# Optimization experiments

Hardware: AMD Instinct MI355X
Metric: run time of the kernel (lower is better)

Reference implementation:

```python
import jax, jax.numpy as jnp
import numpy as np

B, T_D, T_P = 64, 256, 1024
DRUG_DIM, PROT_DIM, D = 128, 128, 128
MAX_LEN = 1024
NEG = -1e9


def _linear_params(k, out_d, in_d):
    k1, k2 = jax.random.split(k)
    lim = 1.0 / np.sqrt(in_d)
    W = jax.random.uniform(k1, (out_d, in_d), minval=-lim, maxval=lim, dtype=jnp.float32)
    b = jax.random.uniform(k2, (out_d,), minval=-lim, maxval=lim, dtype=jnp.float32)
    return W, b


def setup_inputs() -> dict:
    key = jax.random.key(0)
    ks = jax.random.split(key, 13)
    inp = {
        'smiles_embeddings': jax.random.normal(ks[0], (B, T_D, DRUG_DIM), dtype=jnp.float32),
        'protein_embeddings': jax.random.normal(ks[1], (B, T_P, PROT_DIM), dtype=jnp.float32),
        'smiles_mask': jax.random.randint(ks[2], (B, T_D), 0, 2, dtype=jnp.int32),
        'protein_mask': jax.random.randint(ks[3], (B, T_P), 0, 2, dtype=jnp.int32),
        # torch inits pos_bias to zeros; small random values make the test nontrivial
        'pos_bias': 0.02 * jax.random.normal(ks[4], (MAX_LEN, MAX_LEN), dtype=jnp.float32),
    }
    names = [('Wqd', 'bqd', DRUG_DIM), ('Wkp', 'bkp', PROT_DIM), ('Wvp', 'bvp', PROT_DIM),
             ('Wqp', 'bqp', PROT_DIM), ('Wkd', 'bkd', DRUG_DIM), ('Wvd', 'bvd', DRUG_DIM),
             ('Wpd', 'bpd', D), ('Wpp', 'bpp', D)]
    for i, (wn, bn, in_d) in enumerate(names):
        W, b = _linear_params(ks[5 + i], D, in_d)
        inp[wn] = W
        inp[bn] = b
    return inp


def _lin(x, W, b):
    return x @ W.T + b


def _aft(q, k, v, pb_masked, Wp, bp):
    # q: [B,Ti,D]; k,v: [B,Tj,D]; pb_masked: [B,Ti,Tj]
    max_k = k.max(axis=1, keepdims=True)              # per (b,d) over seq j
    max_pb = pb_masked.max(axis=2, keepdims=True)     # per (b,i) over j
    exp_k = jnp.exp(k - max_k)                        # [B,Tj,D]
    exp_pb = jnp.exp(pb_masked - max_pb)              # [B,Ti,Tj]
    num = jnp.einsum('bij,bjd->bid', exp_pb, exp_k * v)
    den = jnp.einsum('bij,bjd->bid', exp_pb, exp_k)
    y = jax.nn.sigmoid(q) * num / den
    return _lin(y, Wp, bp)


def reference(smiles_embeddings, protein_embeddings, smiles_mask, protein_mask, pos_bias,
              Wqd, bqd, Wkp, bkp, Wvp, bvp, Wqp, bqp, Wkd, bkd, Wvd, bvd, Wpd, bpd, Wpp, bpp):
    Td = smiles_embeddings.shape[1]
    Tp = protein_embeddings.shape[1]
    combined = smiles_mask[:, :, None] * protein_mask[:, None, :]  # [B,Td,Tp]
    pb = pos_bias[:Td, :Tp][None]                                   # [1,Td,Tp]

    # drug queries attend over protein keys/values
    pb_d = jnp.where(combined == 0, NEG, pb)
    y_d = _aft(_lin(smiles_embeddings, Wqd, bqd),
               _lin(protein_embeddings, Wkp, bkp),
               _lin(protein_embeddings, Wvp, bvp), pb_d, Wpd, bpd)

    # protein queries attend over drug keys/values (transposed pos bias)
    pb_p = jnp.where(jnp.swapaxes(combined, 1, 2) == 0, NEG, jnp.swapaxes(pb, 1, 2))
    y_p = _aft(_lin(protein_embeddings, Wqp, bqp),
               _lin(smiles_embeddings, Wkd, bkd),
               _lin(smiles_embeddings, Wvd, bvd), pb_p, Wpp, bpp)

    y_d = jnp.where(smiles_mask[:, :, None] == 0, NEG, y_d).max(axis=1)   # [B,D]
    y_p = jnp.where(protein_mask[:, :, None] == 0, NEG, y_p).max(axis=1)  # [B,D]
    return y_d, y_p
```

## Files before the change

kernel.cpp:

```cpp
#include <hip/hip_runtime.h>
#include <cstdint>
#include <cstddef>

#define NEGV -1e9f

typedef __bf16 bf16x8 __attribute__((ext_vector_type(8)));
typedef float f32x4 __attribute__((ext_vector_type(4)));
typedef unsigned short us4 __attribute__((ext_vector_type(4)));
typedef unsigned short us8 __attribute__((ext_vector_type(8)));

__device__ __forceinline__ unsigned short f2bf(float f) {
  unsigned int u = __float_as_uint(f);
  u += 0x7fffu + ((u >> 16) & 1u);
  return (unsigned short)(u >> 16);
}
__device__ __forceinline__ float bf2f(unsigned short u) {
  return __uint_as_float(((unsigned)u) << 16);
}

__device__ __forceinline__ void gld16(const void* g, void* l) {
  __builtin_amdgcn_global_load_lds(
      (const __attribute__((address_space(1))) unsigned int*)g,
      (__attribute__((address_space(3))) unsigned int*)l, 16, 0, 0);
}

__global__ void prep_kernel(const float* __restrict__ w0, const float* __restrict__ w1,
                            const float* __restrict__ w2, const float* __restrict__ w3,
                            const float* __restrict__ w4, const float* __restrict__ w5,
                            const float* __restrict__ w6, const float* __restrict__ w7,
                            unsigned short* __restrict__ Wbf,
                            const float* __restrict__ pb,
                            unsigned short* __restrict__ epb,
                            unsigned short* __restrict__ epbT,
                            unsigned int* __restrict__ outEnc) {
  __shared__ unsigned short t[32][33];
  const int blk = blockIdx.x, tid = threadIdx.x;
  if (blk < 64) {
    outEnc[blk * 256 + tid] = 0u;
    return;
  }
  if (blk < 192) {
    const float* Ws[8] = {w0, w1, w2, w3, w4, w5, w6, w7};
    int idx = (blk - 64) * 256 + tid;
    int mat = idx >> 12, off = idx & 4095;
    float4 v = *(const float4*)&Ws[mat][(size_t)off * 4];
    us4 p;
    p.x = f2bf(v.x); p.y = f2bf(v.y); p.z = f2bf(v.z); p.w = f2bf(v.w);
    *(us4*)&Wbf[(size_t)mat * 16384 + (size_t)off * 4] = p;
    return;
  }
  const int bid = blk - 192;
  const int j0 = (bid & 31) * 32, i0 = (bid >> 5) * 32;
  const int tx = tid & 31, ty = tid >> 5;
#pragma unroll
  for (int r = 0; r < 4; ++r) {
    int i = i0 + ty + r * 8;
    unsigned short u = f2bf(__expf(pb[(size_t)i * 1024 + j0 + tx]));
    epb[(size_t)i * 1024 + j0 + tx] = u;
    t[ty + r * 8][tx] = u;
  }
  __syncthreads();
#pragma unroll
  for (int r = 0; r < 4; ++r)
    epbT[(size_t)(j0 + ty + r * 8) * 256 + i0 + tx] = t[tx][ty + r * 8];
}

__global__ __launch_bounds__(256) void proj3_all(
    const float* __restrict__ smiles, const float* __restrict__ prot,
    const int* __restrict__ smask, const int* __restrict__ pmask,
    const unsigned short* __restrict__ Wbf,
    const float* __restrict__ bqd, const float* __restrict__ bkd, const float* __restrict__ bvd,
    const float* __restrict__ bqp, const float* __restrict__ bkp, const float* __restrict__ bvp,
    unsigned short* __restrict__ sigQd, unsigned short* __restrict__ eKTd,
    unsigned short* __restrict__ eKVTd,
    unsigned short* __restrict__ sigQp, unsigned short* __restrict__ eKTp,
    unsigned short* __restrict__ eKVTp) {
  __shared__ unsigned short smem[2 * 128 * 72];
  unsigned short* xL = smem;
  const int tid = threadIdx.x;

  const float* X; const int* mask;
  const unsigned short *Wq, *Wk, *Wv;
  const float *bq, *bk_, *bv;
  unsigned short *sigQ, *eKT, *eKVT;
  int T, g0;
  if (blockIdx.x < 256) {
    X = smiles; mask = smask; T = 256; g0 = blockIdx.x * 64;
    Wq = Wbf; Wk = Wbf + 16384; Wv = Wbf + 32768;
    bq = bqd; bk_ = bkd; bv = bvd;
    sigQ = sigQd; eKT = eKTd; eKVT = eKVTd;
  } else {
    X = prot; mask = pmask; T = 1024; g0 = (blockIdx.x - 256) * 64;
    Wq = Wbf + 3 * 16384; Wk = Wbf + 4 * 16384; Wv = Wbf + 5 * 16384;
    bq = bqp; bk_ = bkp; bv = bvp;
    sigQ = sigQp; eKT = eKTp; eKVT = eKVTp;
  }
  const int b = g0 / T;
  const int tl0 = g0 - b * T;

#pragma unroll
  for (int r = 0; r < 8; ++r) {
    int i4 = tid + 256 * r;
    int t = i4 >> 5, k4 = (i4 & 31) * 4;
    float4 v = *(const float4*)&X[(size_t)(g0 + t) * 128 + k4];
    us4 p;
    p.x = f2bf(v.x); p.y = f2bf(v.y); p.z = f2bf(v.z); p.w = f2bf(v.w);
    *(us4*)&xL[t * 136 + k4] = p;
  }
  __syncthreads();

  const int lane = tid & 63, wave = tid >> 6;
  const int lo = lane & 15, hi = lane >> 4;
  const int d0 = wave * 32;

  f32x4 aQ[4][2], aK[4][2], aV[4][2];
#pragma unroll
  for (int a = 0; a < 4; ++a)
#pragma unroll
    for (int s = 0; s < 2; ++s)
#pragma unroll
      for (int r = 0; r < 4; ++r) { aQ[a][s][r] = 0.f; aK[a][s][r] = 0.f; aV[a][s][r] = 0.f; }

#pragma unroll
  for (int kt = 0; kt < 128; kt += 32) {
    bf16x8 bQ[2], bK[2], bV[2];
#pragma unroll
    for (int s = 0; s < 2; ++s) {
      size_t roff = (size_t)(d0 + s * 16 + lo) * 128 + kt + hi * 8;
      bQ[s] = *(const bf16x8*)&Wq[roff];
      bK[s] = *(const bf16x8*)&Wk[roff];
      bV[s] = *(const bf16x8*)&Wv[roff];
    }
#pragma unroll
    for (int a = 0; a < 4; ++a) {
      bf16x8 af = *(const bf16x8*)&xL[(a * 16 + lo) * 136 + kt + hi * 8];
#pragma unroll
      for (int s = 0; s < 2; ++s) {
        aQ[a][s] = __builtin_amdgcn_mfma_f32_16x16x32_bf16(af, bQ[s], aQ[a][s], 0, 0, 0);
        aK[a][s] = __builtin_amdgcn_mfma_f32_16x16x32_bf16(af, bK[s], aK[a][s], 0, 0, 0);
        aV[a][s] = __builtin_amdgcn_mfma_f32_16x16x32_bf16(af, bV[s], aV[a][s], 0, 0, 0);
      }
    }
  }

#pragma unroll
  for (int s = 0; s < 2; ++s) {
    int d = d0 + s * 16 + lo;
    float bb = bq[d];
#pragma unroll
    for (int a = 0; a < 4; ++a)
#pragma unroll
      for (int r = 0; r < 4; ++r) {
        int t = g0 + a * 16 + hi * 4 + r;
        float q = aQ[a][s][r] + bb;
        sigQ[(size_t)t * 128 + d] = f2bf(1.f / (1.f + __expf(-q)));
      }
  }

  __syncthreads();
  unsigned short* ekL = smem;
  unsigned short* ekvL = smem + 9216;
#pragma unroll
  for (int s = 0; s < 2; ++s) {
    int d = d0 + s * 16 + lo;
    float bbk = bk_[d], bbv = bv[d];
#pragma unroll
    for (int a = 0; a < 4; ++a)
#pragma unroll
      for (int r = 0; r < 4; ++r) {
        int tl = a * 16 + hi * 4 + r;
        int mk = mask[g0 + tl];
        float ek = mk ? __expf(aK[a][s][r] + bbk) : 0.f;
        float ekv = ek * (aV[a][s][r] + bbv);
        ekL[d * 72 + tl] = f2bf(ek);
        ekvL[d * 72 + tl] = f2bf(ekv);
      }
  }
  __syncthreads();
#pragma unroll
  for (int r = 0; r < 8; ++r) {
    int q = tid + 256 * r;
    int arr = q >> 10, qq = q & 1023;
    int d = qq >> 3, c = qq & 7;
    us8 v = *(const us8*)&smem[arr * 9216 + d * 72 + c * 8];
    unsigned short* dst = arr ? eKVT : eKT;
    *(us8*)&dst[((size_t)b * 128 + d) * T + tl0 + c * 8] = v;
  }
}

__global__ __launch_bounds__(256, 2) void aft_all(
    const unsigned short* __restrict__ epb, const unsigned short* __restrict__ epbT,
    const unsigned short* __restrict__ eKTd, const unsigned short* __restrict__ eKVTd,
    const unsigned short* __restrict__ eKTp, const unsigned short* __restrict__ eKVTp,
    const unsigned short* __restrict__ sigQd, const unsigned short* __restrict__ sigQp,
    const int* __restrict__ smask, const int* __restrict__ pmask,
    const unsigned short* __restrict__ Wbf,
    const float* __restrict__ bpd, const float* __restrict__ bpp,
    unsigned int* __restrict__ outEnc) {
  __shared__ unsigned short smem[32768];

  const int blk = blockIdx.x;
  const unsigned short *Ap, *KT, *VT, *SQ, *Wp;
  const float* bp;
  const int* msk;
  unsigned int* oEnc;
  int b, i0, TJ, Ti, astr;
  if (blk < 128) {
    b = blk & 63; i0 = (blk >> 6) * 128; TJ = 1024; Ti = 256;
    Ap = epb; astr = 1024; KT = eKTp; VT = eKVTp; SQ = sigQd;
    Wp = Wbf + 6 * 16384; bp = bpd; msk = smask + b * 256 + i0; oEnc = outEnc;
  } else {
    int k = blk - 128;
    b = k & 63; i0 = (k >> 6) * 128; TJ = 256; Ti = 1024;
    Ap = epbT; astr = 256; KT = eKTd; VT = eKVTd; SQ = sigQp;
    Wp = Wbf + 7 * 16384; bp = bpp; msk = pmask + b * 1024 + i0; oEnc = outEnc + 8192;
  }

  const int tid = threadIdx.x, lane = tid & 63, w = tid >> 6;
  const int lo = lane & 15, hi = lane >> 4;
  const int wi = (w >> 1) * 64, wd = (w & 1) * 64;
  const unsigned short* KTb = KT + (size_t)b * 128 * TJ;
  const unsigned short* VTb = VT + (size_t)b * 128 * TJ;
  const int slotbase = w * 256;

  auto stage = [&](int jt, int p) {
    unsigned short* bkL = smem + p * 16384;
    unsigned short* bvL = bkL + 8192;
#pragma unroll
    for (int it = 0; it < 4; ++it) {
      int slot = slotbase + it * 64 + lane;
      int r = slot >> 3, sc = slot & 7;
      int cg = sc ^ (r & 7);
      size_t goff = (size_t)r * TJ + jt + cg * 8;
      gld16(KTb + goff, &bkL[(slotbase + it * 64) * 8]);
      gld16(VTb + goff, &bvL[(slotbase + it * 64) * 8]);
    }
  };

  f32x4 aN[4][4], aD[4][4];
#pragma unroll
  for (int a = 0; a < 4; ++a)
#pragma unroll
    for (int n = 0; n < 4; ++n)
#pragma unroll
      for (int r = 0; r < 4; ++r) { aN[a][n][r] = 0.f; aD[a][n][r] = 0.f; }

  stage(0, 0);
  bf16x8 af_cur[4][2];
#pragma unroll
  for (int a = 0; a < 4; ++a)
#pragma unroll
    for (int kt = 0; kt < 2; ++kt)
      af_cur[a][kt] = *(const bf16x8*)
          &Ap[(size_t)(i0 + wi + a * 16 + lo) * astr + kt * 32 + hi * 8];

  int p = 0;
  for (int jt = 0; jt < TJ; jt += 64) {
    const int jn = (jt + 64 < TJ) ? jt + 64 : jt;
    stage(jn, p ^ 1);
    bf16x8 af_nxt[4][2];
#pragma unroll
    for (int a = 0; a < 4; ++a)
#pragma unroll
      for (int kt = 0; kt < 2; ++kt)
        af_nxt[a][kt] = *(const bf16x8*)
            &Ap[(size_t)(i0 + wi + a * 16 + lo) * astr + jn + kt * 32 + hi * 8];
    asm volatile("s_waitcnt vmcnt(16)\ns_barrier" ::: "memory");

    const unsigned short* bkL = smem + p * 16384;
    const unsigned short* bvL = bkL + 8192;
#pragma unroll
    for (int kt = 0; kt < 2; ++kt) {
      bf16x8 bk[4], bv[4];
#pragma unroll
      for (int n = 0; n < 4; ++n) {
        int row = wd + n * 16 + lo;
        int sc = ((kt * 4 + hi) ^ (row & 7)) * 8;
        bk[n] = *(const bf16x8*)&bkL[row * 64 + sc];
        bv[n] = *(const bf16x8*)&bvL[row * 64 + sc];
      }
#pragma unroll
      for (int a = 0; a < 4; ++a)
#pragma unroll
        for (int n = 0; n < 4; ++n) {
          aN[a][n] = __builtin_amdgcn_mfma_f32_16x16x32_bf16(af_cur[a][kt], bv[n], aN[a][n], 0, 0, 0);
          aD[a][n] = __builtin_amdgcn_mfma_f32_16x16x32_bf16(af_cur[a][kt], bk[n], aD[a][n], 0, 0, 0);
        }
    }
    asm volatile("s_waitcnt lgkmcnt(0)\ns_barrier" ::: "memory");
#pragma unroll
    for (int a = 0; a < 4; ++a)
#pragma unroll
      for (int kt = 0; kt < 2; ++kt)
        af_cur[a][kt] = af_nxt[a][kt];
    p ^= 1;
  }

  __syncthreads();
  unsigned short* yL = smem;
#pragma unroll
  for (int a = 0; a < 4; ++a)
#pragma unroll
    for (int n = 0; n < 4; ++n) {
      int iL = wi + a * 16 + hi * 4;
      int d = wd + n * 16 + lo;
#pragma unroll
      for (int r = 0; r < 4; ++r) {
        size_t off = ((size_t)b * Ti + i0 + iL + r) * 128 + d;
        float s = bf2f(SQ[off]);
        float y = s * __fdividef(aN[a][n][r], aD[a][n][r]);
        yL[(iL + r) * 136 + d] = f2bf(y);
      }
    }
  __syncthreads();

  f32x4 aZ[4][4];
#pragma unroll
  for (int a = 0; a < 4; ++a)
#pragma unroll
    for (int n = 0; n < 4; ++n)
#pragma unroll
      for (int r = 0; r < 4; ++r) aZ[a][n][r] = 0.f;

#pragma unroll
  for (int kt = 0; kt < 128; kt += 32) {
    bf16x8 bw[4];
#pragma unroll
    for (int n = 0; n < 4; ++n)
      bw[n] = *(const bf16x8*)&Wp[(size_t)(wd + n * 16 + lo) * 128 + kt + hi * 8];
#pragma unroll
    for (int a = 0; a < 4; ++a) {
      bf16x8 af = *(const bf16x8*)&yL[(wi + a * 16 + lo) * 136 + kt + hi * 8];
#pragma unroll
      for (int n = 0; n < 4; ++n)
        aZ[a][n] = __builtin_amdgcn_mfma_f32_16x16x32_bf16(af, bw[n], aZ[a][n], 0, 0, 0);
    }
  }

#pragma unroll
  for (int n = 0; n < 4; ++n) {
    int d = wd + n * 16 + lo;
    float bb = bp[d];
    float m = NEGV;
#pragma unroll
    for (int a = 0; a < 4; ++a)
#pragma unroll
      for (int r = 0; r < 4; ++r) {
        int iL = wi + a * 16 + hi * 4 + r;
        float z = aZ[a][n][r] + bb;
        m = msk[iL] ? fmaxf(m, z) : m;
      }
    m = fmaxf(m, __shfl_xor(m, 16, 64));
    m = fmaxf(m, __shfl_xor(m, 32, 64));
    if (hi == 0) {
      unsigned bits = __float_as_uint(m);
      unsigned key = (bits & 0x80000000u) ? ~bits : (bits | 0x80000000u);
      atomicMax(&oEnc[b * 128 + d], key);
    }
  }
}

__global__ void out_decode(unsigned int* o) {
  int i = blockIdx.x * 256 + threadIdx.x;
  unsigned k = o[i];
  unsigned bits = (k & 0x80000000u) ? (k ^ 0x80000000u) : ~k;
  ((float*)o)[i] = __uint_as_float(bits);
}

extern "C" void kernel_launch(void* const* d_in, const int* in_sizes, int n_in,
                              void* d_out, int out_size, void* d_ws, size_t ws_size,
                              hipStream_t stream) {
  const float* smiles = (const float*)d_in[0];
  const float* prot   = (const float*)d_in[1];
  const int* smask = (const int*)d_in[2];
  const int* pmask = (const int*)d_in[3];
  const float* pos_bias = (const float*)d_in[4];
  const float* Wqd = (const float*)d_in[5];  const float* bqd = (const float*)d_in[6];
  const float* Wkp = (const float*)d_in[7];  const float* bkp = (const float*)d_in[8];
  const float* Wvp = (const float*)d_in[9];  const float* bvp = (const float*)d_in[10];
  const float* Wqp = (const float*)d_in[11]; const float* bqp = (const float*)d_in[12];
  const float* Wkd = (const float*)d_in[13]; const float* bkd = (const float*)d_in[14];
  const float* Wvd = (const float*)d_in[15]; const float* bvd = (const float*)d_in[16];
  const float* Wpd = (const float*)d_in[17]; const float* bpd = (const float*)d_in[18];
  const float* Wpp = (const float*)d_in[19]; const float* bpp = (const float*)d_in[20];

  unsigned short* u = (unsigned short*)d_ws;
  unsigned short* eKTp  = u;
  unsigned short* eKVTp = eKTp + 8388608;
  unsigned short* eKTd  = eKVTp + 8388608;
  unsigned short* eKVTd = eKTd + 2097152;
  unsigned short* sigQd = eKVTd + 2097152;
  unsigned short* sigQp = sigQd + 2097152;
  unsigned short* epb_  = sigQp + 8388608;
  unsigned short* epbT_ = epb_ + 262144;
  unsigned short* Wbf   = epbT_ + 262144;

  dim3 blk(256);

  prep_kernel<<<448, blk, 0, stream>>>(Wqd, Wkd, Wvd, Wqp, Wkp, Wvp, Wpd, Wpp,
                                       Wbf, pos_bias, epb_, epbT_,
                                       (unsigned int*)d_out);

  proj3_all<<<1280, blk, 0, stream>>>(smiles, prot, smask, pmask, Wbf,
                                      bqd, bkd, bvd, bqp, bkp, bvp,
                                      sigQd, eKTd, eKVTd, sigQp, eKTp, eKVTp);

  aft_all<<<640, blk, 0, stream>>>(epb_, epbT_, eKTd, eKVTd, eKTp, eKVTp,
                                   sigQd, sigQp, smask, pmask, Wbf,
                                   bpd, bpp, (unsigned int*)d_out);

  out_decode<<<64, blk, 0, stream>>>((unsigned int*)d_out);
}
```

Measured before the change: 196.5 us.

## Pre-swizzle operands into MFMA fragment layout and drop LDS staging in AFT

The projection kernel now writes sigmoid(Q), exp(K) and exp(K)*V directly in MFMA-fragment-ordered layouts, and extra blocks reorder the exp(pos_bias) matrices the same way. The AFT kernel then loads each operand fragment straight from global memory with contiguous 16-byte loads. This replaces the double-buffered LDS pipeline with its barriers and the LDS transpose pass in the projection kernel. The cost is that the main loop no longer overlaps prefetch explicitly and relies on cache and occupancy to hide global latency. B fragments are also re-read from global memory by each wave instead of being shared through LDS.

```diff
diff --git a/kernel.cpp b/kernel.cpp
--- a/kernel.cpp
+++ b/kernel.cpp
@@ -18,11 +18,6 @@
   return __uint_as_float(((unsigned)u) << 16);
 }
 
-__device__ __forceinline__ void gld16(const void* g, void* l) {
-  __builtin_amdgcn_global_load_lds(
-      (const __attribute__((address_space(1))) unsigned int*)g,
-      (__attribute__((address_space(3))) unsigned int*)l, 16, 0, 0);
-}
 
 __global__ void prep_kernel(const float* __restrict__ w0, const float* __restrict__ w1,
                             const float* __restrict__ w2, const float* __restrict__ w3,
@@ -71,32 +66,50 @@
     const unsigned short* __restrict__ Wbf,
     const float* __restrict__ bqd, const float* __restrict__ bkd, const float* __restrict__ bvd,
     const float* __restrict__ bqp, const float* __restrict__ bkp, const float* __restrict__ bvp,
-    unsigned short* __restrict__ sigQd, unsigned short* __restrict__ eKTd,
-    unsigned short* __restrict__ eKVTd,
-    unsigned short* __restrict__ sigQp, unsigned short* __restrict__ eKTp,
-    unsigned short* __restrict__ eKVTp) {
-  __shared__ unsigned short smem[2 * 128 * 72];
-  unsigned short* xL = smem;
+    const unsigned short* __restrict__ epb, const unsigned short* __restrict__ epbT,
+    unsigned short* __restrict__ AFd, unsigned short* __restrict__ AFp,
+    unsigned short* __restrict__ SQd, unsigned short* __restrict__ BKd,
+    unsigned short* __restrict__ BVd,
+    unsigned short* __restrict__ SQp, unsigned short* __restrict__ BKp,
+    unsigned short* __restrict__ BVp) {
   const int tid = threadIdx.x;
+
+  if (blockIdx.x >= 1280) {
+    int sid = (blockIdx.x - 1280) * 256 + tid;
+    if (sid < 32768) {
+      int lane = sid & 63, kt = (sid >> 6) & 31, it = sid >> 11;
+      int i = it * 16 + (lane & 15), j = kt * 32 + (lane >> 4) * 8;
+      *(us8*)&AFd[(size_t)sid * 8] = *(const us8*)&epb[(size_t)i * 1024 + j];
+    } else {
+      int s2 = sid - 32768;
+      int lane = s2 & 63, kt = (s2 >> 6) & 7, it = s2 >> 9;
+      int i = it * 16 + (lane & 15), j = kt * 32 + (lane >> 4) * 8;
+      *(us8*)&AFp[(size_t)s2 * 8] = *(const us8*)&epbT[(size_t)i * 256 + j];
+    }
+    return;
+  }
+
+  __shared__ unsigned short xL[64 * 136];
 
   const float* X; const int* mask;
   const unsigned short *Wq, *Wk, *Wv;
   const float *bq, *bk_, *bv;
-  unsigned short *sigQ, *eKT, *eKVT;
+  unsigned short *SQ, *BK, *BV;
   int T, g0;
   if (blockIdx.x < 256) {
     X = smiles; mask = smask; T = 256; g0 = blockIdx.x * 64;
     Wq = Wbf; Wk = Wbf + 16384; Wv = Wbf + 32768;
     bq = bqd; bk_ = bkd; bv = bvd;
-    sigQ = sigQd; eKT = eKTd; eKVT = eKVTd;
+    SQ = SQd; BK = BKd; BV = BVd;
   } else {
     X = prot; mask = pmask; T = 1024; g0 = (blockIdx.x - 256) * 64;
     Wq = Wbf + 3 * 16384; Wk = Wbf + 4 * 16384; Wv = Wbf + 5 * 16384;
     bq = bqp; bk_ = bkp; bv = bvp;
-    sigQ = sigQp; eKT = eKTp; eKVT = eKVTp;
+    SQ = SQp; BK = BKp; BV = BVp;
   }
   const int b = g0 / T;
   const int tl0 = g0 - b * T;
+  const int NIT = T / 16, NKT = T / 32;
 
 #pragma unroll
   for (int r = 0; r < 8; ++r) {
@@ -145,97 +158,83 @@
 
 #pragma unroll
   for (int s = 0; s < 2; ++s) {
-    int d = d0 + s * 16 + lo;
-    float bb = bq[d];
-#pragma unroll
-    for (int a = 0; a < 4; ++a)
+    int dt = (d0 >> 4) + s;
+    float bb = bq[d0 + s * 16 + lo];
+#pragma unroll
+    for (int a = 0; a < 4; ++a) {
+      int it = (tl0 >> 4) + a;
+      us4 v;
 #pragma unroll
       for (int r = 0; r < 4; ++r) {
-        int t = g0 + a * 16 + hi * 4 + r;
         float q = aQ[a][s][r] + bb;
-        sigQ[(size_t)t * 128 + d] = f2bf(1.f / (1.f + __expf(-q)));
-      }
-  }
-
-  __syncthreads();
-  unsigned short* ekL = smem;
-  unsigned short* ekvL = smem + 9216;
+        v[r] = f2bf(1.f / (1.f + __expf(-q)));
+      }
+      ((us4*)SQ)[(((size_t)b * NIT + it) * 8 + dt) * 64 + lane] = v;
+    }
+  }
+
 #pragma unroll
   for (int s = 0; s < 2; ++s) {
-    int d = d0 + s * 16 + lo;
-    float bbk = bk_[d], bbv = bv[d];
-#pragma unroll
-    for (int a = 0; a < 4; ++a)
+    int dt = (d0 >> 4) + s;
+    float bbk = bk_[d0 + s * 16 + lo], bbv = bv[d0 + s * 16 + lo];
+#pragma unroll
+    for (int a = 0; a < 4; ++a) {
+      int kt = (tl0 >> 5) + (a >> 1);
+      int lane_f = ((a & 1) * 2 + (hi >> 1)) * 16 + lo;
+      us4 vk, vv;
 #pragma unroll
       for (int r = 0; r < 4; ++r) {
-        int tl = a * 16 + hi * 4 + r;
-        int mk = mask[g0 + tl];
+        int tg = g0 + a * 16 + hi * 4 + r;
+        int mk = mask[tg];
         float ek = mk ? __expf(aK[a][s][r] + bbk) : 0.f;
         float ekv = ek * (aV[a][s][r] + bbv);
-        ekL[d * 72 + tl] = f2bf(ek);
-        ekvL[d * 72 + tl] = f2bf(ekv);
-      }
-  }
-  __syncthreads();
-#pragma unroll
-  for (int r = 0; r < 8; ++r) {
-    int q = tid + 256 * r;
-    int arr = q >> 10, qq = q & 1023;
-    int d = qq >> 3, c = qq & 7;
-    us8 v = *(const us8*)&smem[arr * 9216 + d * 72 + c * 8];
-    unsigned short* dst = arr ? eKVT : eKT;
-    *(us8*)&dst[((size_t)b * 128 + d) * T + tl0 + c * 8] = v;
+        vk[r] = f2bf(ek);
+        vv[r] = f2bf(ekv);
+      }
+      size_t q4 = ((((size_t)b * NKT + kt) * 8 + dt) * 64 + lane_f) * 2 + (hi & 1);
+      ((us4*)BK)[q4] = vk;
+      ((us4*)BV)[q4] = vv;
+    }
   }
 }
 
 __global__ __launch_bounds__(256, 2) void aft_all(
-    const unsigned short* __restrict__ epb, const unsigned short* __restrict__ epbT,
-    const unsigned short* __restrict__ eKTd, const unsigned short* __restrict__ eKVTd,
-    const unsigned short* __restrict__ eKTp, const unsigned short* __restrict__ eKVTp,
-    const unsigned short* __restrict__ sigQd, const unsigned short* __restrict__ sigQp,
+    const unsigned short* __restrict__ AFd, const unsigned short* __restrict__ AFp,
+    const unsigned short* __restrict__ SQd, const unsigned short* __restrict__ BKd,
+    const unsigned short* __restrict__ BVd,
+    const unsigned short* __restrict__ SQp, const unsigned short* __restrict__ BKp,
+    const unsigned short* __restrict__ BVp,
     const int* __restrict__ smask, const int* __restrict__ pmask,
     const unsigned short* __restrict__ Wbf,
     const float* __restrict__ bpd, const float* __restrict__ bpp,
     unsigned int* __restrict__ outEnc) {
-  __shared__ unsigned short smem[32768];
+  __shared__ unsigned short yL[128 * 136];
 
   const int blk = blockIdx.x;
-  const unsigned short *Ap, *KT, *VT, *SQ, *Wp;
+  const unsigned short *AF, *BK, *BV, *SQ, *Wp;
   const float* bp;
   const int* msk;
   unsigned int* oEnc;
-  int b, i0, TJ, Ti, astr;
+  int b, i0, NKT, NIT;
   if (blk < 128) {
-    b = blk & 63; i0 = (blk >> 6) * 128; TJ = 1024; Ti = 256;
-    Ap = epb; astr = 1024; KT = eKTp; VT = eKVTp; SQ = sigQd;
+    b = blk & 63; i0 = (blk >> 6) * 128; NKT = 32; NIT = 16;
+    AF = AFd; BK = BKp; BV = BVp; SQ = SQd;
     Wp = Wbf + 6 * 16384; bp = bpd; msk = smask + b * 256 + i0; oEnc = outEnc;
   } else {
     int k = blk - 128;
-    b = k & 63; i0 = (k >> 6) * 128; TJ = 256; Ti = 1024;
-    Ap = epbT; astr = 256; KT = eKTd; VT = eKVTd; SQ = sigQp;
+    b = k & 63; i0 = (k >> 6) * 128; NKT = 8; NIT = 64;
+    AF = AFp; BK = BKd; BV = BVd; SQ = SQp;
     Wp = Wbf + 7 * 16384; bp = bpp; msk = pmask + b * 1024 + i0; oEnc = outEnc + 8192;
   }
 
   const int tid = threadIdx.x, lane = tid & 63, w = tid >> 6;
   const int lo = lane & 15, hi = lane >> 4;
   const int wi = (w >> 1) * 64, wd = (w & 1) * 64;
-  const unsigned short* KTb = KT + (size_t)b * 128 * TJ;
-  const unsigned short* VTb = VT + (size_t)b * 128 * TJ;
-  const int slotbase = w * 256;
-
-  auto stage = [&](int jt, int p) {
-    unsigned short* bkL = smem + p * 16384;
-    unsigned short* bvL = bkL + 8192;
-#pragma unroll
-    for (int it = 0; it < 4; ++it) {
-      int slot = slotbase + it * 64 + lane;
-      int r = slot >> 3, sc = slot & 7;
-      int cg = sc ^ (r & 7);
-      size_t goff = (size_t)r * TJ + jt + cg * 8;
-      gld16(KTb + goff, &bkL[(slotbase + it * 64) * 8]);
-      gld16(VTb + goff, &bvL[(slotbase + it * 64) * 8]);
-    }
-  };
+  const int it0 = (i0 + wi) >> 4;
+  const int dt0 = wd >> 4;
+
+  const unsigned short* BKb = BK + (size_t)b * NKT * 8 * 64 * 8;
+  const unsigned short* BVb = BV + (size_t)b * NKT * 8 * 64 * 8;
 
   f32x4 aN[4][4], aD[4][4];
 #pragma unroll
@@ -245,70 +244,38 @@
 #pragma unroll
       for (int r = 0; r < 4; ++r) { aN[a][n][r] = 0.f; aD[a][n][r] = 0.f; }
 
-  stage(0, 0);
-  bf16x8 af_cur[4][2];
+#pragma unroll 2
+  for (int kt = 0; kt < NKT; ++kt) {
+    bf16x8 af[4];
+#pragma unroll
+    for (int a = 0; a < 4; ++a)
+      af[a] = *(const bf16x8*)&AF[(((size_t)(it0 + a) * NKT + kt) * 64 + lane) * 8];
+    bf16x8 bk[4], bv[4];
+#pragma unroll
+    for (int n = 0; n < 4; ++n) {
+      size_t x = (((size_t)kt * 8 + dt0 + n) * 64 + lane) * 8;
+      bk[n] = *(const bf16x8*)&BKb[x];
+      bv[n] = *(const bf16x8*)&BVb[x];
+    }
+#pragma unroll
+    for (int a = 0; a < 4; ++a)
+#pragma unroll
+      for (int n = 0; n < 4; ++n) {
+        aN[a][n] = __builtin_amdgcn_mfma_f32_16x16x32_bf16(af[a], bv[n], aN[a][n], 0, 0, 0);
+        aD[a][n] = __builtin_amdgcn_mfma_f32_16x16x32_bf16(af[a], bk[n], aD[a][n], 0, 0, 0);
+      }
+  }
+
 #pragma unroll
   for (int a = 0; a < 4; ++a)
 #pragma unroll
-    for (int kt = 0; kt < 2; ++kt)
-      af_cur[a][kt] = *(const bf16x8*)
-          &Ap[(size_t)(i0 + wi + a * 16 + lo) * astr + kt * 32 + hi * 8];
-
-  int p = 0;
-  for (int jt = 0; jt < TJ; jt += 64) {
-    const int jn = (jt + 64 < TJ) ? jt + 64 : jt;
-    stage(jn, p ^ 1);
-    bf16x8 af_nxt[4][2];
-#pragma unroll
-    for (int a = 0; a < 4; ++a)
-#pragma unroll
-      for (int kt = 0; kt < 2; ++kt)
-        af_nxt[a][kt] = *(const bf16x8*)
-            &Ap[(size_t)(i0 + wi + a * 16 + lo) * astr + jn + kt * 32 + hi * 8];
-    asm volatile("s_waitcnt vmcnt(16)\ns_barrier" ::: "memory");
-
-    const unsigned short* bkL = smem + p * 16384;
-    const unsigned short* bvL = bkL + 8192;
-#pragma unroll
-    for (int kt = 0; kt < 2; ++kt) {
-      bf16x8 bk[4], bv[4];
-#pragma unroll
-      for (int n = 0; n < 4; ++n) {
-        int row = wd + n * 16 + lo;
-        int sc = ((kt * 4 + hi) ^ (row & 7)) * 8;
-        bk[n] = *(const bf16x8*)&bkL[row * 64 + sc];
-        bv[n] = *(const bf16x8*)&bvL[row * 64 + sc];
-      }
-#pragma unroll
-      for (int a = 0; a < 4; ++a)
-#pragma unroll
-        for (int n = 0; n < 4; ++n) {
-          aN[a][n] = __builtin_amdgcn_mfma_f32_16x16x32_bf16(af_cur[a][kt], bv[n], aN[a][n], 0, 0, 0);
-          aD[a][n] = __builtin_amdgcn_mfma_f32_16x16x32_bf16(af_cur[a][kt], bk[n], aD[a][n], 0, 0, 0);
-        }
-    }
-    asm volatile("s_waitcnt lgkmcnt(0)\ns_barrier" ::: "memory");
-#pragma unroll
-    for (int a = 0; a < 4; ++a)
-#pragma unroll
-      for (int kt = 0; kt < 2; ++kt)
-        af_cur[a][kt] = af_nxt[a][kt];
-    p ^= 1;
-  }
-
-  __syncthreads();
-  unsigned short* yL = smem;
-#pragma unroll
-  for (int a = 0; a < 4; ++a)
-#pragma unroll
     for (int n = 0; n < 4; ++n) {
+      us4 q = ((const us4*)SQ)[(((size_t)b * NIT + it0 + a) * 8 + dt0 + n) * 64 + lane];
       int iL = wi + a * 16 + hi * 4;
       int d = wd + n * 16 + lo;
 #pragma unroll
       for (int r = 0; r < 4; ++r) {
-        size_t off = ((size_t)b * Ti + i0 + iL + r) * 128 + d;
-        float s = bf2f(SQ[off]);
-        float y = s * __fdividef(aN[a][n][r], aD[a][n][r]);
+        float y = bf2f(q[r]) * __fdividef(aN[a][n][r], aD[a][n][r]);
         yL[(iL + r) * 136 + d] = f2bf(y);
       }
     }
@@ -385,15 +352,17 @@
   const float* Wpp = (const float*)d_in[19]; const float* bpp = (const float*)d_in[20];
 
   unsigned short* u = (unsigned short*)d_ws;
-  unsigned short* eKTp  = u;
-  unsigned short* eKVTp = eKTp + 8388608;
-  unsigned short* eKTd  = eKVTp + 8388608;
-  unsigned short* eKVTd = eKTd + 2097152;
-  unsigned short* sigQd = eKVTd + 2097152;
-  unsigned short* sigQp = sigQd + 2097152;
-  unsigned short* epb_  = sigQp + 8388608;
+  unsigned short* BKp_  = u;
+  unsigned short* BVp_  = BKp_ + 8388608;
+  unsigned short* BKd_  = BVp_ + 8388608;
+  unsigned short* BVd_  = BKd_ + 2097152;
+  unsigned short* SQd_  = BVd_ + 2097152;
+  unsigned short* SQp_  = SQd_ + 2097152;
+  unsigned short* epb_  = SQp_ + 8388608;
   unsigned short* epbT_ = epb_ + 262144;
-  unsigned short* Wbf   = epbT_ + 262144;
+  unsigned short* AFd_  = epbT_ + 262144;
+  unsigned short* AFp_  = AFd_ + 262144;
+  unsigned short* Wbf   = AFp_ + 262144;
 
   dim3 blk(256);
 
@@ -401,12 +370,13 @@
                                        Wbf, pos_bias, epb_, epbT_,
                                        (unsigned int*)d_out);
 
-  proj3_all<<<1280, blk, 0, stream>>>(smiles, prot, smask, pmask, Wbf,
+  proj3_all<<<1536, blk, 0, stream>>>(smiles, prot, smask, pmask, Wbf,
                                       bqd, bkd, bvd, bqp, bkp, bvp,
-                                      sigQd, eKTd, eKVTd, sigQp, eKTp, eKVTp);
-
-  aft_all<<<640, blk, 0, stream>>>(epb_, epbT_, eKTd, eKVTd, eKTp, eKVTp,
-                                   sigQd, sigQp, smask, pmask, Wbf,
+                                      epb_, epbT_, AFd_, AFp_,
+                                      SQd_, BKd_, BVd_, SQp_, BKp_, BVp_);
+
+  aft_all<<<640, blk, 0, stream>>>(AFd_, AFp_, SQd_, BKd_, BVd_,
+                                   SQp_, BKp_, BVp_, smask, pmask, Wbf,
                                    bpd, bpp, (unsigned int*)d_out);
 
   out_decode<<<64, blk, 0, stream>>>((unsigned int*)d_out);
```

After: 181.6 us. -7.6%, faster.
